# Optimization experiments

Hardware: AMD Instinct MI355X
Metric: run time of the kernel (lower is better)

## Reference

```python
import jax, jax.numpy as jnp
import numpy as np

B, T, C = 2, 2048, 2048
H, HD = 16, 128          # n_head, head_dim
LORA = C // 4            # kv_lora_rank = n_embd // compression_ratio
RD = HD // 2             # qk_rope_dim
ND = HD - RD             # qk_nope_dim
THETA = 100000.0


def setup_inputs() -> dict:
    key = jax.random.key(0)
    k0, k1, k2, k3, k4 = jax.random.split(key, 5)
    s = 0.02
    return {
        "x": jax.random.normal(k0, (B, T, C), dtype=jnp.float32),
        "Wq": jax.random.normal(k1, (C, H * HD), dtype=jnp.float32) * s,
        "Wkva": jax.random.normal(k2, (C, LORA + RD), dtype=jnp.float32) * s,
        "Wkvb": jax.random.normal(k3, (LORA, H * ND), dtype=jnp.float32) * s,
        "Wo": jax.random.normal(k4, (H * HD, C), dtype=jnp.float32) * s,
    }


def apply_rope(x, theta=THETA):
    # x: [B, H, T, D] with D even; interleaved complex rotation (torch.view_as_complex style)
    b, h, t, d = x.shape
    freqs = 1.0 / (theta ** (jnp.arange(0, d, 2, dtype=jnp.float32) / d))  # [D/2]
    ang = jnp.arange(t, dtype=jnp.float32)[:, None] * freqs[None, :]       # [T, D/2]
    cos, sin = jnp.cos(ang), jnp.sin(ang)
    xr = x.reshape(b, h, t, d // 2, 2)
    x0, x1 = xr[..., 0], xr[..., 1]
    o0 = x0 * cos - x1 * sin
    o1 = x0 * sin + x1 * cos
    return jnp.stack([o0, o1], axis=-1).reshape(b, h, t, d)


def reference(x, Wq, Wkva, Wkvb, Wo):
    Bx, Tx, Cx = x.shape
    # query projection -> [B, H, T, HD]
    q = (x @ Wq).reshape(Bx, Tx, H, HD).transpose(0, 2, 1, 3)
    # compressed KV + shared (MQA) rope key
    ckv = x @ Wkva                                  # [B, T, LORA+RD]
    kv_latent = ckv[..., :LORA]                     # [B, T, LORA]
    k_rope = ckv[..., LORA:]                        # [B, T, RD]
    # decompress nope part of K (== nope part of V)
    kv = (kv_latent @ Wkvb).reshape(Bx, Tx, H, ND).transpose(0, 2, 1, 3)  # [B,H,T,ND]
    k_rope = jnp.broadcast_to(k_rope[:, None, :, :], (Bx, H, Tx, RD))
    q_nope, q_rope = q[..., :ND], q[..., ND:]
    q_rope = apply_rope(q_rope)
    k_rope = apply_rope(k_rope)
    qf = jnp.concatenate([q_nope, q_rope], axis=-1)               # [B,H,T,HD]
    kf = jnp.concatenate([kv, k_rope], axis=-1)                   # [B,H,T,HD]
    vf = jnp.concatenate([kv, jnp.zeros_like(k_rope)], axis=-1)   # [B,H,T,HD]
    scale = 1.0 / np.sqrt(HD).astype(np.float32)
    att = jnp.einsum("bhtd,bhsd->bhts", qf, kf) * scale           # [B,H,T,T]
    causal = jnp.tril(jnp.ones((Tx, Tx), dtype=bool))
    att = jnp.where(causal, att, -jnp.inf)
    att = jax.nn.softmax(att, axis=-1)
    y = jnp.einsum("bhts,bhsd->bhtd", att, vf)                    # [B,H,T,HD]
    y = y.transpose(0, 2, 1, 3).reshape(Bx, Tx, H * HD)
    return y @ Wo
```

## Files before the change

### kernel.cpp

```cpp
#include <hip/hip_runtime.h>
#include <hip/hip_bf16.h>
#include <math.h>

#define B_ 2
#define T_ 2048
#define C_ 2048
#define H_ 16
#define HD_ 128
#define LORA_ 512
#define RD_ 64
#define ND_ 64
#define BT_ (B_*T_)
#define NKVA_ 576
#define NKVAP_ 640
#define LOG2_THETA 16.609640474436812f

typedef __bf16 bf16x8 __attribute__((ext_vector_type(8)));
typedef float  f32x4  __attribute__((ext_vector_type(4)));

#define MFMA16(a,b,c) __builtin_amdgcn_mfma_f32_16x16x32_bf16((a),(b),(c),0,0,0)

__device__ static inline void load_lds16(const __bf16* g, __bf16* l) {
  auto* lp = (__attribute__((address_space(3))) char*)(uintptr_t)(l);
  auto* gp = (const __attribute__((address_space(1))) char*)(g);
  __builtin_amdgcn_global_load_lds(gp, lp, 16, 0, 0);
}

__device__ static inline unsigned pkbf(float a, float b) {
  union { __bf16 h[2]; unsigned u; } v;
  v.h[0] = (__bf16)a; v.h[1] = (__bf16)b;
  return v.u;
}

__global__ __launch_bounds__(256) void k_cast_x(const float* __restrict__ x,
                                                __bf16* __restrict__ xb, int n) {
  int idx = blockIdx.x * 256 + threadIdx.x;
  if (idx < n) xb[idx] = (__bf16)x[idx];
}

__global__ __launch_bounds__(256) void k_tcast(const float* __restrict__ src,
                                               __bf16* __restrict__ dst,
                                               int K, int N, int NP) {
  __shared__ float tile[32][33];
  int k0 = blockIdx.x * 32;
  int n0 = blockIdx.y * 32;
  int tx = threadIdx.x & 31, ty = threadIdx.x >> 5;
  for (int i = ty; i < 32; i += 8) {
    int n = n0 + tx;
    tile[i][tx] = (n < N) ? src[(size_t)(k0 + i) * N + n] : 0.0f;
  }
  __syncthreads();
  for (int i = ty; i < 32; i += 8) {
    dst[(size_t)(n0 + i) * K + k0 + tx] = (__bf16)tile[tx][i];
  }
}

__global__ __launch_bounds__(256) void k_tcast_wo(const float* __restrict__ Wo,
                                                  __bf16* __restrict__ dst) {
  __shared__ float tile[32][33];
  int kc0 = blockIdx.x * 32;
  int n0  = blockIdx.y * 32;
  int rbase = (kc0 >> 6) * 128 + (kc0 & 63);
  int tx = threadIdx.x & 31, ty = threadIdx.x >> 5;
  for (int i = ty; i < 32; i += 8)
    tile[i][tx] = Wo[(size_t)(rbase + i) * C_ + n0 + tx];
  __syncthreads();
  for (int i = ty; i < 32; i += 8)
    dst[(size_t)(n0 + i) * 1024 + kc0 + tx] = (__bf16)tile[tx][i];
}

__global__ __launch_bounds__(256) void k_gemm_bt(const __bf16* __restrict__ A,
                                                 const __bf16* __restrict__ B,
                                                 float* __restrict__ C,
                                                 int M, int N, int K) {
  __shared__ __align__(16) __bf16 As[2][128 * 32];
  __shared__ __align__(16) __bf16 Bs[2][128 * 32];
  const int tid  = threadIdx.x;
  const int lane = tid & 63;
  const int wave = tid >> 6;
  const int bm = blockIdx.x, bn = blockIdx.y;
  const int r0 = tid >> 2;
  const int c8 = (tid & 3) * 8;
  const __bf16* Ag = A + (size_t)(bm * 128 + r0) * K + c8;
  const __bf16* Bg = B + (size_t)(bn * 128 + r0) * K + c8;
  const int wr = (wave >> 1) * 64, wc = (wave & 1) * 64;
  const int fr = lane & 15, fk = (lane >> 4) * 8;
  const f32x4 fzero = {0.f, 0.f, 0.f, 0.f};
  f32x4 acc[4][4];
#pragma unroll
  for (int i = 0; i < 4; ++i)
#pragma unroll
    for (int j = 0; j < 4; ++j) acc[i][j] = fzero;

  load_lds16(Ag,                  &As[0][tid * 8]);
  load_lds16(Ag + (size_t)64 * K, &As[0][tid * 8 + 2048]);
  load_lds16(Bg,                  &Bs[0][tid * 8]);
  load_lds16(Bg + (size_t)64 * K, &Bs[0][tid * 8 + 2048]);

  int buf = 0;
  for (int k0 = 0; k0 < K; k0 += 32) {
    __syncthreads();
    if (k0 + 32 < K) {
      const int nb = buf ^ 1;
      load_lds16(Ag + k0 + 32,                  &As[nb][tid * 8]);
      load_lds16(Ag + (size_t)64 * K + k0 + 32, &As[nb][tid * 8 + 2048]);
      load_lds16(Bg + k0 + 32,                  &Bs[nb][tid * 8]);
      load_lds16(Bg + (size_t)64 * K + k0 + 32, &Bs[nb][tid * 8 + 2048]);
    }
    bf16x8 af[4], bfg[4];
#pragma unroll
    for (int i = 0; i < 4; ++i) af[i]  = *(const bf16x8*)&As[buf][(wr + i * 16 + fr) * 32 + fk];
#pragma unroll
    for (int j = 0; j < 4; ++j) bfg[j] = *(const bf16x8*)&Bs[buf][(wc + j * 16 + fr) * 32 + fk];
#pragma unroll
    for (int i = 0; i < 4; ++i)
#pragma unroll
      for (int j = 0; j < 4; ++j)
        acc[i][j] = MFMA16(af[i], bfg[j], acc[i][j]);
    buf ^= 1;
  }
  const int rbase = (lane >> 4) * 4;
  float* Cb = C + (size_t)(bm * 128 + wr + rbase) * N + bn * 128 + wc + fr;
#pragma unroll
  for (int i = 0; i < 4; ++i)
#pragma unroll
    for (int j = 0; j < 4; ++j)
#pragma unroll
      for (int r = 0; r < 4; ++r)
        Cb[(size_t)(i * 16 + r) * N + j * 16] = acc[i][j][r];
}

__global__ __launch_bounds__(256) void k_rope_q(const float* __restrict__ q,
                                                __bf16* __restrict__ qf) {
  int idx = blockIdx.x * 256 + threadIdx.x;
  int d  = idx & 127;
  int t  = (idx >> 7) & 2047;
  int bh = idx >> 18;
  int h  = bh & 15, b = bh >> 4;
  const float* qrow = q + ((size_t)(b * T_ + t)) * 2048 + h * 128;
  float v;
  if (d < 64) {
    v = qrow[d];
  } else {
    int i = (d - 64) >> 1;
    float freq = exp2f(-((float)(2 * i) / 64.0f) * LOG2_THETA);
    float ang = (float)t * freq;
    float c = cosf(ang), s = sinf(ang);
    float x0 = qrow[64 + 2 * i], x1 = qrow[64 + 2 * i + 1];
    v = (d & 1) ? (x0 * s + x1 * c) : (x0 * c - x1 * s);
  }
  qf[idx] = (__bf16)v;
}

__global__ __launch_bounds__(256) void k_rope_kf(const float* __restrict__ ckv,
                                                 __bf16* __restrict__ kf) {
  int idx = blockIdx.x * 256 + threadIdx.x;
  int d = idx & 63;
  int t = (idx >> 6) & 2047;
  int h = (idx >> 17) & 15;
  int b = idx >> 21;
  const float* src = ckv + ((size_t)(b * T_ + t)) * NKVAP_ + 512;
  int i = d >> 1;
  float freq = exp2f(-((float)(2 * i) / 64.0f) * LOG2_THETA);
  float ang = (float)t * freq;
  float c = cosf(ang), s = sinf(ang);
  float x0 = src[2 * i], x1 = src[2 * i + 1];
  float v = (d & 1) ? (x0 * s + x1 * c) : (x0 * c - x1 * s);
  kf[(((size_t)(b * H_ + h)) * T_ + t) * 128 + 64 + d] = (__bf16)v;
}

__global__ __launch_bounds__(256) void k_cast_kvl(const float* __restrict__ ckv,
                                                  __bf16* __restrict__ kvl) {
  int idx = blockIdx.x * 256 + threadIdx.x;
  int r = idx >> 9, c = idx & 511;
  kvl[idx] = (__bf16)ckv[(size_t)r * NKVAP_ + c];
}

__global__ __launch_bounds__(256) void k_pack_kv(const float* __restrict__ kv,
                                                 __bf16* __restrict__ kf,
                                                 __bf16* __restrict__ kvT) {
  __shared__ float tile[64][65];
  const int bh = blockIdx.x;
  const int b = bh >> 4, h = bh & 15;
  const int t0 = blockIdx.y * 64;
  const int tid = threadIdx.x;
  const int i0 = tid >> 4, d4 = (tid & 15) * 4;
#pragma unroll
  for (int p = 0; p < 4; ++p) {
    int i = i0 + p * 16;
    const float* src = kv + ((size_t)(b * T_ + t0 + i)) * 1024 + h * 64 + d4;
    float4 v = *(const float4*)src;
    tile[i][d4] = v.x; tile[i][d4 + 1] = v.y; tile[i][d4 + 2] = v.z; tile[i][d4 + 3] = v.w;
    union { __bf16 hh[4]; uint2 u; } o;
    o.hh[0] = (__bf16)v.x; o.hh[1] = (__bf16)v.y; o.hh[2] = (__bf16)v.z; o.hh[3] = (__bf16)v.w;
    *(uint2*)(kf + ((size_t)bh * T_ + t0 + i) * 128 + d4) = o.u;
  }
  __syncthreads();
  const int dd = tid >> 2, tc0 = (tid & 3) * 16;
  __bf16 outv[16];
#pragma unroll
  for (int j = 0; j < 16; ++j) outv[j] = (__bf16)tile[tc0 + j][dd];
  __bf16* dst = kvT + ((size_t)(bh * 64 + dd)) * T_ + t0 + tc0;
  *(bf16x8*)dst = *(bf16x8*)&outv[0];
  *(bf16x8*)(dst + 8) = *(bf16x8*)&outv[8];
}

__global__ __launch_bounds__(256, 4) void k_attn(const __bf16* __restrict__ qf,
                                                 const __bf16* __restrict__ kf,
                                                 const __bf16* __restrict__ kvT,
                                                 __bf16* __restrict__ yc) {
  const int blk = blockIdx.x;
  const int bh = blk & 31;
  const int qt = 31 - (blk >> 5);
  const int b = bh >> 4, h = bh & 15;
  const int qbase = qt * 64;
  const int tid = threadIdx.x;
  const int lane = tid & 63, wave = tid >> 6;
  const int fr = lane & 15, quad = lane >> 4, fk8 = quad * 8;

  __shared__ __align__(16) __bf16 Ks[64][136];
  __shared__ __align__(16) __bf16 VsT[64][72];

  const int qi = qbase + wave * 16 + fr;
  const __bf16* qb = qf + ((size_t)bh * T_ + qi) * HD_;
  bf16x8 aq[4];
#pragma unroll
  for (int g = 0; g < 4; ++g) aq[g] = *(const bf16x8*)(qb + g * 32 + fk8);

  const f32x4 fzero = {0.f, 0.f, 0.f, 0.f};
  f32x4 accO[4];
#pragma unroll
  for (int g = 0; g < 4; ++g) accO[g] = fzero;
  float m = -1e30f, l = 0.f;

  const float scale2 = 1.4426950408889634f / sqrtf(128.0f);
  const int srow = tid >> 4, scol = (tid & 15) * 8;
  const int vrow = tid >> 3, vcol = (tid & 7) * 8;
  const __bf16* kbh = kf + (size_t)bh * T_ * 128;
  const __bf16* vbh = kvT + (size_t)bh * 64 * T_;
  const int srcA = (quad & 1) * 32 + fr, srcB = srcA + 16;
  const int hi = quad >> 1;

  for (int s0 = 0; s0 <= qbase; s0 += 64) {
    __syncthreads();
#pragma unroll
    for (int p = 0; p < 4; ++p)
      *(bf16x8*)&Ks[srow + p * 16][scol] =
        *(const bf16x8*)(kbh + (size_t)(s0 + srow + p * 16) * 128 + scol);
#pragma unroll
    for (int p = 0; p < 2; ++p)
      *(bf16x8*)&VsT[vrow + p * 32][vcol] =
        *(const bf16x8*)(vbh + (size_t)(vrow + p * 32) * T_ + s0 + vcol);
    __syncthreads();

    f32x4 accST[4];
#pragma unroll
    for (int cg = 0; cg < 4; ++cg) accST[cg] = fzero;
#pragma unroll
    for (int cg = 0; cg < 4; ++cg) {
#pragma unroll
      for (int kg = 0; kg < 4; ++kg) {
        bf16x8 bk = *(const bf16x8*)&Ks[cg * 16 + fr][kg * 32 + fk8];
        accST[cg] = MFMA16(bk, aq[kg], accST[cg]);
      }
    }

    float lmax = -1e30f;
#pragma unroll
    for (int cg = 0; cg < 4; ++cg) {
#pragma unroll
      for (int r = 0; r < 4; ++r) {
        const int key = s0 + cg * 16 + quad * 4 + r;
        float v = accST[cg][r] * scale2;
        v = (key <= qi) ? v : -1e30f;
        accST[cg][r] = v;
        lmax = fmaxf(lmax, v);
      }
    }
    lmax = fmaxf(lmax, __shfl_xor(lmax, 16, 64));
    lmax = fmaxf(lmax, __shfl_xor(lmax, 32, 64));
    const float mn = fmaxf(m, lmax);
    const float alpha = exp2f(m - mn);
    m = mn;

    float lsum = 0.f;
    unsigned pk0[4], pk1[4];
#pragma unroll
    for (int cg = 0; cg < 4; ++cg) {
      float p0 = exp2f(accST[cg][0] - m);
      float p1 = exp2f(accST[cg][1] - m);
      float p2 = exp2f(accST[cg][2] - m);
      float p3 = exp2f(accST[cg][3] - m);
      lsum += (p0 + p1) + (p2 + p3);
      pk0[cg] = pkbf(p0, p1);
      pk1[cg] = pkbf(p2, p3);
    }
    lsum += __shfl_xor(lsum, 16, 64);
    lsum += __shfl_xor(lsum, 32, 64);
    l = l * alpha + lsum;
#pragma unroll
    for (int g = 0; g < 4; ++g)
#pragma unroll
      for (int r = 0; r < 4; ++r) accO[g][r] *= alpha;

#pragma unroll
    for (int ks = 0; ks < 2; ++ks) {
      int a0 = __shfl((int)pk0[2 * ks], srcA, 64);
      int b0 = __shfl((int)pk0[2 * ks + 1], srcA, 64);
      int a1 = __shfl((int)pk1[2 * ks], srcA, 64);
      int b1 = __shfl((int)pk1[2 * ks + 1], srcA, 64);
      int a2 = __shfl((int)pk0[2 * ks], srcB, 64);
      int b2 = __shfl((int)pk0[2 * ks + 1], srcB, 64);
      int a3 = __shfl((int)pk1[2 * ks], srcB, 64);
      int b3 = __shfl((int)pk1[2 * ks + 1], srcB, 64);
      union { int i[4]; bf16x8 v; } pf;
      pf.i[0] = hi ? b0 : a0;
      pf.i[1] = hi ? b1 : a1;
      pf.i[2] = hi ? b2 : a2;
      pf.i[3] = hi ? b3 : a3;
#pragma unroll
      for (int g = 0; g < 4; ++g) {
        bf16x8 vv = *(const bf16x8*)&VsT[g * 16 + fr][ks * 32 + fk8];
        accO[g] = MFMA16(vv, pf.v, accO[g]);
      }
    }
  }

  const float linv = 1.0f / l;
  __bf16* yb = yc + ((size_t)(b * T_ + qi)) * 1024 + h * 64 + quad * 4;
#pragma unroll
  for (int g = 0; g < 4; ++g) {
    union { unsigned u[2]; uint2 v; } o;
    o.u[0] = pkbf(accO[g][0] * linv, accO[g][1] * linv);
    o.u[1] = pkbf(accO[g][2] * linv, accO[g][3] * linv);
    *(uint2*)(yb + g * 16) = o.v;
  }
}

extern "C" void kernel_launch(void* const* d_in, const int* in_sizes, int n_in,
                              void* d_out, int out_size, void* d_ws, size_t ws_size,
                              hipStream_t stream) {
  const float* x    = (const float*)d_in[0];
  const float* Wq   = (const float*)d_in[1];
  const float* Wkva = (const float*)d_in[2];
  const float* Wkvb = (const float*)d_in[3];
  const float* Wo   = (const float*)d_in[4];
  float* out = (float*)d_out;
  char* ws = (char*)d_ws;

  size_t off = 0;
  __bf16* xb    = (__bf16*)(ws + off); off += (size_t)BT_ * C_ * 2;
  __bf16* WqT   = (__bf16*)(ws + off); off += (size_t)2048 * 2048 * 2;
  __bf16* WkvaT = (__bf16*)(ws + off); off += (size_t)NKVAP_ * 2048 * 2;
  __bf16* WkvbT = (__bf16*)(ws + off); off += (size_t)1024 * 512 * 2;
  __bf16* WoTc  = (__bf16*)(ws + off); off += (size_t)2048 * 1024 * 2;
  float*  q     = (float*)(ws + off);  off += (size_t)BT_ * 2048 * 4;
  float*  ckv   = (float*)(ws + off);  off += (size_t)BT_ * NKVAP_ * 4;
  __bf16* kvl   = (__bf16*)(ws + off); off += (size_t)BT_ * 512 * 2;
  float*  kv    = (float*)(ws + off);  off += (size_t)BT_ * 1024 * 4;
  __bf16* qfb   = (__bf16*)(ws + off); off += (size_t)B_ * H_ * T_ * HD_ * 2;
  __bf16* yc    = (__bf16*)(ws + off); off += (size_t)BT_ * 1024 * 2;
  __bf16* kfb = (__bf16*)q;
  __bf16* kvT = (__bf16*)((char*)q + (size_t)B_ * H_ * T_ * HD_ * 2);

  k_cast_x<<<(BT_ * C_) / 256, 256, 0, stream>>>(x, xb, BT_ * C_);
  k_tcast<<<dim3(2048 / 32, 2048 / 32), 256, 0, stream>>>(Wq, WqT, 2048, 2048, 2048);
  k_tcast<<<dim3(2048 / 32, NKVAP_ / 32), 256, 0, stream>>>(Wkva, WkvaT, 2048, NKVA_, NKVAP_);
  k_tcast<<<dim3(512 / 32, 1024 / 32), 256, 0, stream>>>(Wkvb, WkvbT, 512, 1024, 1024);
  k_tcast_wo<<<dim3(1024 / 32, 2048 / 32), 256, 0, stream>>>(Wo, WoTc);

  k_gemm_bt<<<dim3(BT_ / 128, 2048 / 128), 256, 0, stream>>>(xb, WqT, q, BT_, 2048, 2048);
  k_gemm_bt<<<dim3(BT_ / 128, NKVAP_ / 128), 256, 0, stream>>>(xb, WkvaT, ckv, BT_, NKVAP_, 2048);

  k_rope_q<<<(B_ * H_ * T_ * HD_) / 256, 256, 0, stream>>>(q, qfb);
  k_cast_kvl<<<(BT_ * 512) / 256, 256, 0, stream>>>(ckv, kvl);

  k_gemm_bt<<<dim3(BT_ / 128, 1024 / 128), 256, 0, stream>>>(kvl, WkvbT, kv, BT_, 1024, 512);
  k_pack_kv<<<dim3(B_ * H_, T_ / 64), 256, 0, stream>>>(kv, kfb, kvT);
  k_rope_kf<<<(B_ * H_ * T_ * 64) / 256, 256, 0, stream>>>(ckv, kfb);

  k_attn<<<(T_ / 64) * B_ * H_, 256, 0, stream>>>(qfb, kfb, kvT, yc);

  k_gemm_bt<<<dim3(BT_ / 128, 2048 / 128), 256, 0, stream>>>(yc, WoTc, out, BT_, 2048, 1024);
}
```

Before: 350.7 us.

## Prefetch next K/V tile into registers and fold softmax scale into Q

The attention kernel now loads the next K/V tile from global memory into registers while computing on the current LDS tile, so global latency overlaps the MFMA work. The softmax scale (with log2e) is folded into Q during the RoPE kernel, and causal masking runs only on the diagonal tile. s_setprio is raised around the MFMA blocks to favour matrix issue. This adds register pressure and rounds Q after scaling in bf16, which changes precision slightly.

New measurement: 348.8 us. About the same (-0.5%).

```diff
diff --git a/kernel.cpp b/kernel.cpp
--- a/kernel.cpp
+++ b/kernel.cpp
@@ -132,6 +132,7 @@
 
 __global__ __launch_bounds__(256) void k_rope_q(const float* __restrict__ q,
                                                 __bf16* __restrict__ qf) {
+  const float scale2 = 1.4426950408889634f / 11.313708498984760f;
   int idx = blockIdx.x * 256 + threadIdx.x;
   int d  = idx & 127;
   int t  = (idx >> 7) & 2047;
@@ -149,7 +150,7 @@
     float x0 = qrow[64 + 2 * i], x1 = qrow[64 + 2 * i + 1];
     v = (d & 1) ? (x0 * s + x1 * c) : (x0 * c - x1 * s);
   }
-  qf[idx] = (__bf16)v;
+  qf[idx] = (__bf16)(v * scale2);
 }
 
 __global__ __launch_bounds__(256) void k_rope_kf(const float* __restrict__ ckv,
@@ -233,7 +234,6 @@
   for (int g = 0; g < 4; ++g) accO[g] = fzero;
   float m = -1e30f, l = 0.f;
 
-  const float scale2 = 1.4426950408889634f / sqrtf(128.0f);
   const int srow = tid >> 4, scol = (tid & 15) * 8;
   const int vrow = tid >> 3, vcol = (tid & 7) * 8;
   const __bf16* kbh = kf + (size_t)bh * T_ * 128;
@@ -241,21 +241,36 @@
   const int srcA = (quad & 1) * 32 + fr, srcB = srcA + 16;
   const int hi = quad >> 1;
 
+  bf16x8 kreg[4], vreg[2];
+#pragma unroll
+  for (int p = 0; p < 4; ++p)
+    kreg[p] = *(const bf16x8*)(kbh + (size_t)(srow + p * 16) * 128 + scol);
+#pragma unroll
+  for (int p = 0; p < 2; ++p)
+    vreg[p] = *(const bf16x8*)(vbh + (size_t)(vrow + p * 32) * T_ + vcol);
+
   for (int s0 = 0; s0 <= qbase; s0 += 64) {
     __syncthreads();
 #pragma unroll
-    for (int p = 0; p < 4; ++p)
-      *(bf16x8*)&Ks[srow + p * 16][scol] =
-        *(const bf16x8*)(kbh + (size_t)(s0 + srow + p * 16) * 128 + scol);
-#pragma unroll
-    for (int p = 0; p < 2; ++p)
-      *(bf16x8*)&VsT[vrow + p * 32][vcol] =
-        *(const bf16x8*)(vbh + (size_t)(vrow + p * 32) * T_ + s0 + vcol);
+    for (int p = 0; p < 4; ++p) *(bf16x8*)&Ks[srow + p * 16][scol] = kreg[p];
+#pragma unroll
+    for (int p = 0; p < 2; ++p) *(bf16x8*)&VsT[vrow + p * 32][vcol] = vreg[p];
     __syncthreads();
 
+    if (s0 < qbase) {
+      const int sn = s0 + 64;
+#pragma unroll
+      for (int p = 0; p < 4; ++p)
+        kreg[p] = *(const bf16x8*)(kbh + (size_t)(sn + srow + p * 16) * 128 + scol);
+#pragma unroll
+      for (int p = 0; p < 2; ++p)
+        vreg[p] = *(const bf16x8*)(vbh + (size_t)(vrow + p * 32) * T_ + sn + vcol);
+    }
+
     f32x4 accST[4];
 #pragma unroll
     for (int cg = 0; cg < 4; ++cg) accST[cg] = fzero;
+    __builtin_amdgcn_s_setprio(1);
 #pragma unroll
     for (int cg = 0; cg < 4; ++cg) {
 #pragma unroll
@@ -264,17 +279,26 @@
         accST[cg] = MFMA16(bk, aq[kg], accST[cg]);
       }
     }
+    __builtin_amdgcn_s_setprio(0);
 
     float lmax = -1e30f;
-#pragma unroll
-    for (int cg = 0; cg < 4; ++cg) {
-#pragma unroll
-      for (int r = 0; r < 4; ++r) {
-        const int key = s0 + cg * 16 + quad * 4 + r;
-        float v = accST[cg][r] * scale2;
-        v = (key <= qi) ? v : -1e30f;
-        accST[cg][r] = v;
-        lmax = fmaxf(lmax, v);
+    if (s0 == qbase) {
+#pragma unroll
+      for (int cg = 0; cg < 4; ++cg) {
+#pragma unroll
+        for (int r = 0; r < 4; ++r) {
+          const int key = s0 + cg * 16 + quad * 4 + r;
+          float v = accST[cg][r];
+          v = (key <= qi) ? v : -1e30f;
+          accST[cg][r] = v;
+          lmax = fmaxf(lmax, v);
+        }
+      }
+    } else {
+#pragma unroll
+      for (int cg = 0; cg < 4; ++cg) {
+#pragma unroll
+        for (int r = 0; r < 4; ++r) lmax = fmaxf(lmax, accST[cg][r]);
       }
     }
     lmax = fmaxf(lmax, __shfl_xor(lmax, 16, 64));
@@ -318,11 +342,13 @@
       pf.i[1] = hi ? b1 : a1;
       pf.i[2] = hi ? b2 : a2;
       pf.i[3] = hi ? b3 : a3;
+      __builtin_amdgcn_s_setprio(1);
 #pragma unroll
       for (int g = 0; g < 4; ++g) {
         bf16x8 vv = *(const bf16x8*)&VsT[g * 16 + fr][ks * 32 + fk8];
         accO[g] = MFMA16(vv, pf.v, accO[g]);
       }
+      __builtin_amdgcn_s_setprio(0);
     }
   }
 
```
